# Optimization experiments

Hardware: AMD Instinct MI355X
Metric: run time of the kernel (lower is better)

The kernel has to match this reference:

```python
import jax, jax.numpy as jnp
import numpy as np
import math

B, S, D, H = 4, 2048, 1024, 16
HD = D // H  # head dim = 64

def setup_inputs() -> dict:
    key = jax.random.key(0)
    ks = jax.random.split(key, 8)
    scale = 1.0 / math.sqrt(D)
    return {
        "hidden_states": jax.random.normal(ks[0], (B, S, D), jnp.float32),
        "attention_mask": jnp.zeros((B, 1, 1, S), jnp.float32),
        "Wq": jax.random.normal(ks[1], (D, D), jnp.float32) * scale,
        "bq": jnp.zeros((D,), jnp.float32),
        "Wk": jax.random.normal(ks[2], (D, D), jnp.float32) * scale,
        "bk": jnp.zeros((D,), jnp.float32),
        "Wv": jax.random.normal(ks[3], (D, D), jnp.float32) * scale,
        "bv": jnp.zeros((D,), jnp.float32),
    }

def _split_heads(x):
    # [B,S,D] -> [B,H,S,HD]
    return x.reshape(B, S, H, HD).transpose(0, 2, 1, 3)

def reference(hidden_states, attention_mask, Wq, bq, Wk, bk, Wv, bv):
    q = _split_heads(hidden_states @ Wq + bq)
    k = _split_heads(hidden_states @ Wk + bk)
    v = _split_heads(hidden_states @ Wv + bv)
    scores = jnp.einsum("bhqd,bhkd->bhqk", q, k) / math.sqrt(HD)
    scores = scores + attention_mask
    probs = jax.nn.softmax(scores, axis=-1)
    ctx = jnp.einsum("bhqk,bhkd->bhqd", probs, v)
    # [B,H,S,HD] -> [B,S,D]
    return ctx.transpose(0, 2, 1, 3).reshape(B, S, D)
```

## Files before the change

### kernel.cpp

```cpp
#include <hip/hip_runtime.h>
#include <hip/hip_bf16.h>
#include <stdint.h>

#define Bc 4
#define Sc 2048
#define Dc 1024
#define Hc 16
#define HDc 64
#define LOG2E 1.44269504088896f

typedef __attribute__((ext_vector_type(8))) __bf16 bf16x8;
typedef __attribute__((ext_vector_type(4))) __bf16 bf16x4;
typedef __attribute__((ext_vector_type(4))) float f32x4;
typedef __attribute__((ext_vector_type(16))) float f32x16;
typedef __attribute__((ext_vector_type(2))) int i32x2_t;

__device__ __forceinline__ f32x4 mfma16(bf16x8 a, bf16x8 b, f32x4 c) {
  return __builtin_amdgcn_mfma_f32_16x16x32_bf16(a, b, c, 0, 0, 0);
}
__device__ __forceinline__ f32x16 mfma32(bf16x8 a, bf16x8 b, f32x16 c) {
  return __builtin_amdgcn_mfma_f32_32x32x16_bf16(a, b, c, 0, 0, 0);
}
__device__ __forceinline__ uint32_t cvtpk_bf16(float lo, float hi) {
  uint32_t r;
  asm("v_cvt_pk_bf16_f32 %0, %1, %2" : "=v"(r) : "v"(lo), "v"(hi));
  return r;
}
__device__ __forceinline__ void gload_lds16(const void* g, void* l) {
  __builtin_amdgcn_global_load_lds(
      (const __attribute__((address_space(1))) void*)g,
      (__attribute__((address_space(3))) void*)l, 16, 0, 0);
}
__device__ __forceinline__ void gload_lds4(const void* g, void* l) {
  __builtin_amdgcn_global_load_lds(
      (const __attribute__((address_space(1))) void*)g,
      (__attribute__((address_space(3))) void*)l, 4, 0, 0);
}

__global__ __launch_bounds__(256) void maskscale_kernel(const float* __restrict__ m,
                                                        float* __restrict__ mkx) {
  const int i = blockIdx.x * 256 + threadIdx.x;
  mkx[i] = m[i] * LOG2E;
}

__global__ __launch_bounds__(256) void hs2bf_kernel(const float* __restrict__ hs,
                                                    __bf16* __restrict__ Ah) {
  const size_t i = ((size_t)blockIdx.x * 256 + threadIdx.x) * 8;
  float4 f0 = *(const float4*)(hs + i);
  float4 f1 = *(const float4*)(hs + i + 4);
  bf16x8 o;
  o[0] = (__bf16)f0.x; o[1] = (__bf16)f0.y; o[2] = (__bf16)f0.z; o[3] = (__bf16)f0.w;
  o[4] = (__bf16)f1.x; o[5] = (__bf16)f1.y; o[6] = (__bf16)f1.z; o[7] = (__bf16)f1.w;
  *(bf16x8*)(Ah + i) = o;
}

__global__ __launch_bounds__(256) void wtrans_kernel(
    const float* __restrict__ Wq, const float* __restrict__ Wk,
    const float* __restrict__ Wv, __bf16* __restrict__ Wt) {
  const float* W = (blockIdx.z == 0) ? Wq : (blockIdx.z == 1 ? Wk : Wv);
  __bf16* out = Wt + (size_t)blockIdx.z * Dc * Dc;
  const int n0 = blockIdx.x * 64, k0 = blockIdx.y * 64;
  __shared__ float tile[64][65];
  const int tid = threadIdx.x;
  const int r = tid >> 2, cs = (tid & 3) * 16;
  const float* src = W + (size_t)(k0 + r) * Dc + n0 + cs;
  float4 f0 = *(const float4*)(src + 0);
  float4 f1 = *(const float4*)(src + 4);
  float4 f2 = *(const float4*)(src + 8);
  float4 f3 = *(const float4*)(src + 12);
#pragma unroll
  for (int j = 0; j < 4; ++j) {
    tile[r][cs + j] = ((const float*)&f0)[j];
    tile[r][cs + 4 + j] = ((const float*)&f1)[j];
    tile[r][cs + 8 + j] = ((const float*)&f2)[j];
    tile[r][cs + 12 + j] = ((const float*)&f3)[j];
  }
  __syncthreads();
  bf16x8 o0, o1;
#pragma unroll
  for (int j = 0; j < 8; ++j) {
    o0[j] = (__bf16)tile[cs + j][r];
    o1[j] = (__bf16)tile[cs + 8 + j][r];
  }
  __bf16* dst = out + (size_t)(n0 + r) * Dc + k0 + cs;
  *(bf16x8*)(dst) = o0;
  *(bf16x8*)(dst + 8) = o1;
}

__global__ __launch_bounds__(256) void qkv_gemm_kernel(
    const __bf16* __restrict__ A, const __bf16* __restrict__ Wt,
    const float* __restrict__ bq, const float* __restrict__ bk,
    const float* __restrict__ bv,
    __bf16* __restrict__ Qo, __bf16* __restrict__ Kf, __bf16* __restrict__ Vf) {
  const int orig = blockIdx.x;
  const int nt = orig & 7;
  const int rest = orig >> 3;
  const int w = rest >> 6;
  const int mt = rest & 63;
  const int m0 = mt * 128, n0 = nt * 128;

  const __bf16* Bp = Wt + (size_t)w * Dc * Dc;
  const float* bias = (w == 0) ? bq : (w == 1 ? bk : bv);

  __shared__ __attribute__((aligned(16))) __bf16 Asm[2][128 * 32];
  __shared__ __attribute__((aligned(16))) __bf16 Bsm[2][128 * 32];

  const int tid = threadIdx.x, lane = tid & 63, wid = tid >> 6;
  const int wm = wid >> 1, wn = wid & 1;
  const int lg = lane >> 4, li = lane & 15;

  f32x4 acc[4][4] = {};

  auto stage = [&](int buf, int k0) {
#pragma unroll
    for (int i = 0; i < 2; ++i) {
      const int u = i * 256 + tid;
      const int row = u >> 2, c = u & 3;
      const int gc = c ^ (row & 3);
      gload_lds16(A + (size_t)(m0 + row) * Dc + k0 + gc * 8,
                  &Asm[buf][i * 2048 + wid * 512]);
      gload_lds16(Bp + (size_t)(n0 + row) * Dc + k0 + gc * 8,
                  &Bsm[buf][i * 2048 + wid * 512]);
    }
  };

  int cur = 0;
  stage(0, 0);
  __syncthreads();

  for (int k0 = 0; k0 < Dc; k0 += 32) {
    if (k0 + 32 < Dc) stage(cur ^ 1, k0 + 32);
    bf16x8 af[4], bfr[4];
#pragma unroll
    for (int i = 0; i < 4; ++i) {
      const int rowa = wm * 64 + i * 16 + li;
      af[i] = *(const bf16x8*)&Asm[cur][rowa * 32 + (lg ^ (rowa & 3)) * 8];
      const int rowb = wn * 64 + i * 16 + li;
      bfr[i] = *(const bf16x8*)&Bsm[cur][rowb * 32 + (lg ^ (rowb & 3)) * 8];
    }
#pragma unroll
    for (int i = 0; i < 4; ++i)
#pragma unroll
      for (int j = 0; j < 4; ++j)
        acc[i][j] = mfma16(af[i], bfr[j], acc[i][j]);
    __syncthreads();
    cur ^= 1;
  }

  if (w == 0) {
    const float scl = 0.125f * LOG2E;
#pragma unroll
    for (int i = 0; i < 4; ++i) {
#pragma unroll
      for (int j = 0; j < 4; ++j) {
        const int n = n0 + wn * 64 + j * 16 + li;
        const float bb = bias[n];
        const int h = n >> 6, hd = n & 63;
#pragma unroll
        for (int r = 0; r < 4; ++r) {
          const int m = m0 + wm * 64 + i * 16 + lg * 4 + r;
          const int b = m >> 11, s = m & 2047;
          Qo[(((size_t)b * Hc + h) * Sc + s) * HDc + hd] =
              (__bf16)((acc[i][j][r] + bb) * scl);
        }
      }
    }
  } else if (w == 1) {
#pragma unroll
    for (int j = 0; j < 4; ++j) {
      const int n = n0 + wn * 64 + j * 16 + li;
      const float bb = bias[n];
      const int h = n >> 6, hd = n & 63;
      const int c = hd >> 4, shi = (hd >> 3) & 1, j8 = hd & 7;
#pragma unroll
      for (int i = 0; i < 4; ++i) {
#pragma unroll
        for (int r = 0; r < 4; ++r) {
          const int m = m0 + wm * 64 + i * 16 + lg * 4 + r;
          const int b = m >> 11, s = m & 2047;
          const int bh = b * Hc + h;
          const int t = s >> 6, kt = s & 63;
          const int slot = (kt >> 5) * 256 + c * 64 + shi * 32 + (kt & 31);
          Kf[((size_t)(bh * 32 + t)) * 4096 + slot * 8 + j8] =
              (__bf16)(acc[i][j][r] + bb);
        }
      }
    }
  } else {
#pragma unroll
    for (int i = 0; i < 4; ++i) {
      const int mbase = m0 + wm * 64 + i * 16 + lg * 4;
      const int b = mbase >> 11, sk = mbase & 2047;
      const int t = sk >> 6, kt = sk & 63;
      const int kc = kt >> 4, shi = (kt >> 3) & 1, j0 = kt & 7;
#pragma unroll
      for (int j = 0; j < 4; ++j) {
        const int n = n0 + wn * 64 + j * 16 + li;
        const float bb = bias[n];
        const int h = n >> 6, hd = n & 63;
        const int nb = hd >> 5, sqr = hd & 31;
        const int bh = b * Hc + h;
        const int slot = kc * 128 + nb * 64 + shi * 32 + sqr;
        bf16x4 o;
#pragma unroll
        for (int r = 0; r < 4; ++r) o[r] = (__bf16)(acc[i][j][r] + bb);
        *(bf16x4*)&Vf[((size_t)(bh * 32 + t)) * 4096 + slot * 8 + j0] = o;
      }
    }
  }
}

__global__ __launch_bounds__(256) void attn_kernel(
    const __bf16* __restrict__ Q, const __bf16* __restrict__ Kf,
    const __bf16* __restrict__ Vf, const float* __restrict__ mkx,
    float* __restrict__ out) {
  const int qt = blockIdx.x;
  const int bh = blockIdx.y;
  const int b = bh >> 4, h = bh & 15;
  const __bf16* qb = Q + (size_t)bh * Sc * HDc;
  const __bf16* kfb = Kf + (size_t)bh * 32 * 4096;
  const __bf16* vfb = Vf + (size_t)bh * 32 * 4096;
  const float* mb = mkx + (size_t)b * Sc;

  const int tid = threadIdx.x, lane = tid & 63, wid = tid >> 6;
  const int hi = lane >> 5, qr = lane & 31;

  __shared__ __attribute__((aligned(16))) __bf16 Ksm[4][4096];
  __shared__ __attribute__((aligned(16))) __bf16 Vsm[4][4096];
  __shared__ __attribute__((aligned(16))) float Msm[4][64];

  const int q0 = qt * 128 + wid * 32;

  bf16x8 qf[4];
#pragma unroll
  for (int c = 0; c < 4; ++c)
    qf[c] = *(const bf16x8*)(qb + (size_t)(q0 + qr) * HDc + c * 16 + hi * 8);

  bf16x8 onesv;
#pragma unroll
  for (int j = 0; j < 8; ++j) onesv[j] = (__bf16)1.0f;

  f32x16 oacc[2] = {};
  f32x16 lacc = {};
  f32x16 sA[2], sB[2];

  auto stage = [&](int buf, int t) {
    const size_t tb = (size_t)t * 4096;
    gload_lds16(kfb + tb + (size_t)tid * 8, &Ksm[buf][wid * 64 * 8]);
    gload_lds16(vfb + tb + (size_t)tid * 8, &Vsm[buf][wid * 64 * 8]);
    gload_lds16(kfb + tb + (size_t)(256 + tid) * 8, &Ksm[buf][(256 + wid * 64) * 8]);
    gload_lds16(vfb + tb + (size_t)(256 + tid) * 8, &Vsm[buf][(256 + wid * 64) * 8]);
    gload_lds4(mb + t * 64 + lane, &Msm[buf][0]);
  };

  auto qk = [&](int buf, f32x16 (&s)[2]) {
    const __bf16* Kb = &Ksm[buf][0] + lane * 8;
    const float* Mb = &Msm[buf][0];
#pragma unroll
    for (int kb2 = 0; kb2 < 2; ++kb2) {
#pragma unroll
      for (int g = 0; g < 4; ++g) {
        const float4 m4 = *(const float4*)&Mb[kb2 * 32 + g * 8 + hi * 4];
#pragma unroll
        for (int e = 0; e < 4; ++e) s[kb2][g * 4 + e] = ((const float*)&m4)[e];
      }
    }
    __builtin_amdgcn_s_setprio(1);
#pragma unroll
    for (int kb2 = 0; kb2 < 2; ++kb2) {
#pragma unroll
      for (int c = 0; c < 4; ++c) {
        const bf16x8 kf = *(const bf16x8*)(Kb + (kb2 * 4 + c) * 512);
        s[kb2] = mfma32(kf, qf[c], s[kb2]);
      }
    }
    __builtin_amdgcn_s_setprio(0);
  };

  auto softpv = [&](int buf, f32x16 (&s)[2]) {
    const __bf16* Vb = &Vsm[buf][0] + lane * 8;
    bf16x8 pa[4];
#pragma unroll
    for (int kb2 = 0; kb2 < 2; ++kb2) {
      uint32_t wv[8];
#pragma unroll
      for (int j = 0; j < 8; ++j)
        wv[j] = cvtpk_bf16(__builtin_amdgcn_exp2f(s[kb2][2 * j]),
                           __builtin_amdgcn_exp2f(s[kb2][2 * j + 1]));
#pragma unroll
      for (int cc = 0; cc < 2; ++cc) {
        i32x2_t s02 = __builtin_amdgcn_permlane32_swap(
            (int)wv[cc * 4 + 0], (int)wv[cc * 4 + 2], false, false);
        i32x2_t s13 = __builtin_amdgcn_permlane32_swap(
            (int)wv[cc * 4 + 1], (int)wv[cc * 4 + 3], false, false);
        union { uint32_t u[4]; bf16x8 v; } af;
        af.u[0] = (uint32_t)s02[0];
        af.u[1] = (uint32_t)s13[0];
        af.u[2] = (uint32_t)s02[1];
        af.u[3] = (uint32_t)s13[1];
        pa[kb2 * 2 + cc] = af.v;
      }
    }
    __builtin_amdgcn_s_setprio(1);
#pragma unroll
    for (int kc = 0; kc < 4; ++kc) {
      lacc = mfma32(pa[kc], onesv, lacc);
#pragma unroll
      for (int nb = 0; nb < 2; ++nb) {
        const bf16x8 vf = *(const bf16x8*)(Vb + (kc * 2 + nb) * 512);
        oacc[nb] = mfma32(pa[kc], vf, oacc[nb]);
      }
    }
    __builtin_amdgcn_s_setprio(0);
  };

  const int NT = Sc / 64;

  stage(0, 0);
  stage(1, 1);
  stage(2, 2);
  __builtin_amdgcn_sched_barrier(0);
  asm volatile("s_waitcnt vmcnt(10)" ::: "memory");
  __builtin_amdgcn_s_barrier();
  __builtin_amdgcn_sched_barrier(0);
  qk(0, sA);

#define ITER(T, SB, QB, PB, CUR, NXT)                                   \
  {                                                                     \
    const int t_ = (T);                                                 \
    const int tn_ = (t_ + 3 < NT) ? t_ + 3 : NT - 1;                    \
    stage(SB, tn_);                                                     \
    __builtin_amdgcn_sched_barrier(0);                                  \
    asm volatile("s_waitcnt vmcnt(10)" ::: "memory");   \
    __builtin_amdgcn_s_barrier();                                       \
    __builtin_amdgcn_sched_barrier(0);                                  \
    qk(QB, NXT);        \
    softpv(PB, CUR);   \
    __builtin_amdgcn_sched_barrier(0);                                  \
    __builtin_amdgcn_s_barrier();   \
  }

  for (int t4 = 0; t4 < NT; t4 += 4) {
    ITER(t4 + 0, 3, 1, 0, sA, sB);
    ITER(t4 + 1, 0, 2, 1, sB, sA);
    ITER(t4 + 2, 1, 3, 2, sA, sB);
    ITER(t4 + 3, 2, 0, 3, sB, sA);
  }
#undef ITER

  float inv[16];
#pragma unroll
  for (int r = 0; r < 16; ++r) inv[r] = __builtin_amdgcn_rcpf(lacc[r]);
#pragma unroll
  for (int nb = 0; nb < 2; ++nb) {
#pragma unroll
    for (int r = 0; r < 16; ++r) {
      const int row = (r & 3) + 8 * (r >> 2) + 4 * hi;
      const int qg = q0 + row;
      out[((size_t)b * Sc + qg) * Dc + h * HDc + nb * 32 + qr] =
          oacc[nb][r] * inv[r];
    }
  }
}

extern "C" void kernel_launch(void* const* d_in, const int* in_sizes, int n_in,
                              void* d_out, int out_size, void* d_ws,
                              size_t ws_size, hipStream_t stream) {
  const float* hs = (const float*)d_in[0];
  const float* mask = (const float*)d_in[1];
  const float* Wq = (const float*)d_in[2];
  const float* bq = (const float*)d_in[3];
  const float* Wk = (const float*)d_in[4];
  const float* bk = (const float*)d_in[5];
  const float* Wv = (const float*)d_in[6];
  const float* bv = (const float*)d_in[7];
  float* out = (float*)d_out;

  char* ws = (char*)d_ws;
  const size_t qkv_bytes = (size_t)Bc * Hc * Sc * HDc * 2;
  __bf16* Wt = (__bf16*)ws;
  __bf16* Ah = (__bf16*)(ws + 6291456);
  __bf16* Q = (__bf16*)(ws + 6291456 + qkv_bytes);
  __bf16* Kf = (__bf16*)(ws + 6291456 + 2 * qkv_bytes);
  __bf16* Vf = (__bf16*)(ws + 6291456 + 3 * qkv_bytes);
  float* mkx = (float*)(ws + 6291456 + 4 * qkv_bytes);

  maskscale_kernel<<<32, 256, 0, stream>>>(mask, mkx);
  hs2bf_kernel<<<4096, 256, 0, stream>>>(hs, Ah);
  wtrans_kernel<<<dim3(16, 16, 3), 256, 0, stream>>>(Wq, Wk, Wv, Wt);
  qkv_gemm_kernel<<<1536, 256, 0, stream>>>(Ah, Wt, bq, bk, bv, Q, Kf, Vf);
  attn_kernel<<<dim3(16, 64), 256, 0, stream>>>(Q, Kf, Vf, mkx, out);
}
```

Measured before the change: 203.3 us.

## Enlarge QKV GEMM tiles to 128x256 with 512 threads and XCD-aware block remap

```diff
diff --git a/kernel.cpp b/kernel.cpp
--- a/kernel.cpp
+++ b/kernel.cpp
@@ -87,64 +87,75 @@
   *(bf16x8*)(dst + 8) = o1;
 }
 
-__global__ __launch_bounds__(256) void qkv_gemm_kernel(
+__global__ __launch_bounds__(512, 6) void qkv_gemm_kernel(
     const __bf16* __restrict__ A, const __bf16* __restrict__ Wt,
     const float* __restrict__ bq, const float* __restrict__ bk,
     const float* __restrict__ bv,
     __bf16* __restrict__ Qo, __bf16* __restrict__ Kf, __bf16* __restrict__ Vf) {
-  const int orig = blockIdx.x;
-  const int nt = orig & 7;
-  const int rest = orig >> 3;
-  const int w = rest >> 6;
-  const int mt = rest & 63;
-  const int m0 = mt * 128, n0 = nt * 128;
-
-  const __bf16* Bp = Wt + (size_t)w * Dc * Dc;
+  const int wg = (blockIdx.x & 7) * 96 + (blockIdx.x >> 3);
+  const int nn = wg >> 6;
+  const int mm = wg & 63;
+  const int m0 = mm * 128;
+  const int n0 = nn * 256;
+  const int w = n0 >> 10;
+  const int nbase = n0 & 1023;
+
   const float* bias = (w == 0) ? bq : (w == 1 ? bk : bv);
 
-  __shared__ __attribute__((aligned(16))) __bf16 Asm[2][128 * 32];
-  __shared__ __attribute__((aligned(16))) __bf16 Bsm[2][128 * 32];
+  __shared__ __attribute__((aligned(16))) __bf16 Asm[2][4096];
+  __shared__ __attribute__((aligned(16))) __bf16 Bsm[2][8192];
 
   const int tid = threadIdx.x, lane = tid & 63, wid = tid >> 6;
-  const int wm = wid >> 1, wn = wid & 1;
+  const int wr = wid >> 2, wc = wid & 3;
   const int lg = lane >> 4, li = lane & 15;
 
   f32x4 acc[4][4] = {};
 
-  auto stage = [&](int buf, int k0) {
-#pragma unroll
-    for (int i = 0; i < 2; ++i) {
-      const int u = i * 256 + tid;
-      const int row = u >> 2, c = u & 3;
-      const int gc = c ^ (row & 3);
-      gload_lds16(A + (size_t)(m0 + row) * Dc + k0 + gc * 8,
-                  &Asm[buf][i * 2048 + wid * 512]);
-      gload_lds16(Bp + (size_t)(n0 + row) * Dc + k0 + gc * 8,
-                  &Bsm[buf][i * 2048 + wid * 512]);
+  auto stage = [&](int buf, int kt) {
+    const int k0 = kt * 32;
+    {
+      const int row = tid >> 2;
+      const int sc = (tid & 3) ^ (row & 3);
+      gload_lds16(A + (size_t)(m0 + row) * Dc + k0 + sc * 8,
+                  &Asm[buf][wid * 512]);
+    }
+#pragma unroll
+    for (int p = 0; p < 2; ++p) {
+      const int row = p * 128 + (tid >> 2);
+      const int sc = (tid & 3) ^ (row & 3);
+      gload_lds16(Wt + (size_t)(n0 + row) * Dc + k0 + sc * 8,
+                  &Bsm[buf][p * 4096 + wid * 512]);
     }
   };
 
-  int cur = 0;
+  const int aoff = (wr * 64 + li) * 32 + ((lg ^ (li & 3)) * 8);
+  const int boff = (wc * 64 + li) * 32 + ((lg ^ (li & 3)) * 8);
+
   stage(0, 0);
-  __syncthreads();
-
-  for (int k0 = 0; k0 < Dc; k0 += 32) {
-    if (k0 + 32 < Dc) stage(cur ^ 1, k0 + 32);
+  for (int ks = 0; ks < 32; ++ks) {
+    const int tn = (ks + 1 < 32) ? ks + 1 : 31;
+    stage((ks + 1) & 1, tn);
+    __builtin_amdgcn_sched_barrier(0);
+    asm volatile("s_waitcnt vmcnt(3)" ::: "memory");
+    __builtin_amdgcn_s_barrier();
+    __builtin_amdgcn_sched_barrier(0);
+    const __bf16* Ab = &Asm[ks & 1][0] + aoff;
+    const __bf16* Bb = &Bsm[ks & 1][0] + boff;
     bf16x8 af[4], bfr[4];
 #pragma unroll
-    for (int i = 0; i < 4; ++i) {
-      const int rowa = wm * 64 + i * 16 + li;
-      af[i] = *(const bf16x8*)&Asm[cur][rowa * 32 + (lg ^ (rowa & 3)) * 8];
-      const int rowb = wn * 64 + i * 16 + li;
-      bfr[i] = *(const bf16x8*)&Bsm[cur][rowb * 32 + (lg ^ (rowb & 3)) * 8];
-    }
+    for (int i = 0; i < 4; ++i) af[i] = *(const bf16x8*)(Ab + i * 512);
+#pragma unroll
+    for (int j = 0; j < 4; ++j) bfr[j] = *(const bf16x8*)(Bb + j * 512);
+    __builtin_amdgcn_s_setprio(1);
 #pragma unroll
     for (int i = 0; i < 4; ++i)
 #pragma unroll
       for (int j = 0; j < 4; ++j)
         acc[i][j] = mfma16(af[i], bfr[j], acc[i][j]);
-    __syncthreads();
-    cur ^= 1;
+    __builtin_amdgcn_s_setprio(0);
+    asm volatile("" ::: "memory");
+    __builtin_amdgcn_sched_barrier(0);
+    __builtin_amdgcn_s_barrier();
   }
 
   if (w == 0) {
@@ -153,12 +164,12 @@
     for (int i = 0; i < 4; ++i) {
 #pragma unroll
       for (int j = 0; j < 4; ++j) {
-        const int n = n0 + wn * 64 + j * 16 + li;
+        const int n = nbase + wc * 64 + j * 16 + li;
         const float bb = bias[n];
         const int h = n >> 6, hd = n & 63;
 #pragma unroll
         for (int r = 0; r < 4; ++r) {
-          const int m = m0 + wm * 64 + i * 16 + lg * 4 + r;
+          const int m = m0 + wr * 64 + i * 16 + lg * 4 + r;
           const int b = m >> 11, s = m & 2047;
           Qo[(((size_t)b * Hc + h) * Sc + s) * HDc + hd] =
               (__bf16)((acc[i][j][r] + bb) * scl);
@@ -168,7 +179,7 @@
   } else if (w == 1) {
 #pragma unroll
     for (int j = 0; j < 4; ++j) {
-      const int n = n0 + wn * 64 + j * 16 + li;
+      const int n = nbase + wc * 64 + j * 16 + li;
       const float bb = bias[n];
       const int h = n >> 6, hd = n & 63;
       const int c = hd >> 4, shi = (hd >> 3) & 1, j8 = hd & 7;
@@ -176,7 +187,7 @@
       for (int i = 0; i < 4; ++i) {
 #pragma unroll
         for (int r = 0; r < 4; ++r) {
-          const int m = m0 + wm * 64 + i * 16 + lg * 4 + r;
+          const int m = m0 + wr * 64 + i * 16 + lg * 4 + r;
           const int b = m >> 11, s = m & 2047;
           const int bh = b * Hc + h;
           const int t = s >> 6, kt = s & 63;
@@ -189,13 +200,13 @@
   } else {
 #pragma unroll
     for (int i = 0; i < 4; ++i) {
-      const int mbase = m0 + wm * 64 + i * 16 + lg * 4;
+      const int mbase = m0 + wr * 64 + i * 16 + lg * 4;
       const int b = mbase >> 11, sk = mbase & 2047;
       const int t = sk >> 6, kt = sk & 63;
       const int kc = kt >> 4, shi = (kt >> 3) & 1, j0 = kt & 7;
 #pragma unroll
       for (int j = 0; j < 4; ++j) {
-        const int n = n0 + wn * 64 + j * 16 + li;
+        const int n = nbase + wc * 64 + j * 16 + li;
         const float bb = bias[n];
         const int h = n >> 6, hd = n & 63;
         const int nb = hd >> 5, sqr = hd & 31;
@@ -388,6 +399,6 @@
   maskscale_kernel<<<32, 256, 0, stream>>>(mask, mkx);
   hs2bf_kernel<<<4096, 256, 0, stream>>>(hs, Ah);
   wtrans_kernel<<<dim3(16, 16, 3), 256, 0, stream>>>(Wq, Wk, Wv, Wt);
-  qkv_gemm_kernel<<<1536, 256, 0, stream>>>(Ah, Wt, bq, bk, bv, Q, Kf, Vf);
+  qkv_gemm_kernel<<<768, 512, 0, stream>>>(Ah, Wt, bq, bk, bv, Q, Kf, Vf);
   attn_kernel<<<dim3(16, 64), 256, 0, stream>>>(Q, Kf, Vf, mkx, out);
 }
```

New measurement: 511.2 us. +151.5%, slower.
